# Optimization experiments

Measured on AMD Instinct MI355X. Metric: run time of the kernel, lower is better.

The kernel has to match this reference:

```python
import jax, jax.numpy as jnp
import numpy as np

NUM_EXPERTS = 8
TOP_K = 2
D = 2048   # hidden_dim
F = 4096   # ffn_dim


def setup_inputs() -> dict:
    key = jax.random.key(0)
    k0, k1, k2, k3, k4 = jax.random.split(key, 5)
    hidden_states = jax.random.normal(k0, (2, 2048, D), dtype=jnp.float32)
    gate_w = jax.random.normal(k1, (NUM_EXPERTS, D), dtype=jnp.float32) * 0.02
    w1 = jax.random.normal(k2, (NUM_EXPERTS, F, D), dtype=jnp.float32) * 0.02
    w2 = jax.random.normal(k3, (NUM_EXPERTS, D, F), dtype=jnp.float32) * 0.02
    w3 = jax.random.normal(k4, (NUM_EXPERTS, F, D), dtype=jnp.float32) * 0.02
    return {"hidden_states": hidden_states, "gate_w": gate_w, "w1": w1, "w2": w2, "w3": w3}


def reference(hidden_states, gate_w, w1, w2, w3):
    B, S, Dm = hidden_states.shape
    h = hidden_states.reshape(-1, Dm)                      # [T, D]
    router_logits = h @ gate_w.T                           # [T, E]
    rw = jax.nn.softmax(router_logits.astype(jnp.float32), axis=-1)
    rw, selected = jax.lax.top_k(rw, TOP_K)                # [T, K], [T, K]
    rw = rw / jnp.sum(rw, axis=-1, keepdims=True)
    rw = rw.astype(h.dtype)
    final = jnp.zeros_like(h)
    for e in range(NUM_EXPERTS):                            # small fixed loop over experts
        w = jnp.sum(rw * (selected == e), axis=1, keepdims=True)  # [T, 1]
        gated = jax.nn.silu(h @ w1[e].T) * (h @ w3[e].T)   # [T, F]
        final = final + (gated @ w2[e].T) * w              # [T, D]
    return final.reshape(B, S, Dm), router_logits
```

## Files before the change

### kernel.cpp

```cpp
#include <hip/hip_runtime.h>
#include <hip/hip_bf16.h>
#include <stdint.h>

#define NE 8
#define DD 2048
#define FF 4096
#define TT 4096
#define NRB 1024
#define NCV 3072

typedef __attribute__((ext_vector_type(8))) short bf16x8;
typedef __attribute__((ext_vector_type(4))) float f32x4;

__device__ inline unsigned short f2bf(float f) {
  union { float f; unsigned u; } x; x.f = f;
  unsigned r = x.u + 0x7fffu + ((x.u >> 16) & 1u);
  return (unsigned short)(r >> 16);
}
__device__ inline float bf2f(unsigned short v) {
  union { unsigned u; float f; } x; x.u = (unsigned)v << 16; return x.f;
}

__device__ __forceinline__ void convw(const float* __restrict__ src,
                                      unsigned short* __restrict__ dst,
                                      long base, int tid) {
  float4 v[16];
#pragma unroll
  for (int j = 0; j < 16; j++)
    v[j] = *(const float4*)(src + base + j * 1024 + tid * 4);
#pragma unroll
  for (int j = 0; j < 16; j++) {
    ushort4 o;
    o.x = f2bf(v[j].x); o.y = f2bf(v[j].y); o.z = f2bf(v[j].z); o.w = f2bf(v[j].w);
    *(ushort4*)(dst + base + j * 1024 + tid * 4) = o;
  }
}

#define GLL16(g, l) __builtin_amdgcn_global_load_lds( \
    (__attribute__((address_space(1))) void*)(void*)(g), \
    (__attribute__((address_space(3))) void*)(l), 16, 0, 0)

__device__ __forceinline__ void router_one(
    int t, int lane, const float* __restrict__ h, const float* __restrict__ gw,
    float* __restrict__ logits, unsigned short* __restrict__ hb,
    int* __restrict__ counts, int* __restrict__ tok_idx,
    int* __restrict__ sel_e, int* __restrict__ sel_slot, float* __restrict__ sel_w) {
  const float4* hr = (const float4*)(h + (size_t)t * DD);
  float4 hv[8];
  float acc[NE];
#pragma unroll
  for (int e = 0; e < NE; e++) acc[e] = 0.f;
#pragma unroll
  for (int j = 0; j < 8; j++) hv[j] = hr[j * 64 + lane];
  ushort4* hbr = (ushort4*)(hb + (size_t)t * DD);
#pragma unroll
  for (int j = 0; j < 8; j++) {
    ushort4 o;
    o.x = f2bf(hv[j].x); o.y = f2bf(hv[j].y); o.z = f2bf(hv[j].z); o.w = f2bf(hv[j].w);
    hbr[j * 64 + lane] = o;
  }
#pragma unroll
  for (int e = 0; e < NE; e++) {
    const float4* g = (const float4*)(gw + (size_t)e * DD);
    float a = 0.f;
#pragma unroll
    for (int j = 0; j < 8; j++) {
      float4 gv = g[j * 64 + lane];
      a += hv[j].x * gv.x + hv[j].y * gv.y + hv[j].z * gv.z + hv[j].w * gv.w;
    }
    acc[e] = a;
  }
#pragma unroll
  for (int e = 0; e < NE; e++) {
    float v = acc[e];
#pragma unroll
    for (int o = 32; o > 0; o >>= 1) v += __shfl_xor(v, o, 64);
    acc[e] = v;
  }
  if (lane == 0) {
#pragma unroll
    for (int e = 0; e < NE; e++) logits[(size_t)t * NE + e] = acc[e];
    int e1 = 0; float m1 = acc[0];
#pragma unroll
    for (int e = 1; e < NE; e++) if (acc[e] > m1) { m1 = acc[e]; e1 = e; }
    int e2 = -1; float m2 = -3.4e38f;
#pragma unroll
    for (int e = 0; e < NE; e++) if (e != e1 && acc[e] > m2) { m2 = acc[e]; e2 = e; }
    float s = expf(m2 - m1);
    float wa = 1.f / (1.f + s);
    float wb = s * wa;
    int s1 = atomicAdd(&counts[e1], 1);
    tok_idx[e1 * TT + s1] = t;
    int s2 = atomicAdd(&counts[e2], 1);
    tok_idx[e2 * TT + s2] = t;
    sel_e[2 * t] = e1; sel_slot[2 * t] = s1; sel_w[2 * t] = wa;
    sel_e[2 * t + 1] = e2; sel_slot[2 * t + 1] = s2; sel_w[2 * t + 1] = wb;
  }
}

__global__ __launch_bounds__(256) void prep_kernel(
    const float* __restrict__ h, const float* __restrict__ gw,
    float* __restrict__ logits, unsigned short* __restrict__ hb,
    int* __restrict__ counts, int* __restrict__ tok_idx,
    int* __restrict__ sel_e, int* __restrict__ sel_slot, float* __restrict__ sel_w,
    const float* __restrict__ w1, unsigned short* __restrict__ w1b,
    const float* __restrict__ w3, unsigned short* __restrict__ w3b,
    const float* __restrict__ w2, unsigned short* __restrict__ w2b) {
  int b = blockIdx.x;
  int tid = threadIdx.x;
  if (b < NRB) {
    router_one(b * 4 + (tid >> 6), tid & 63,
               h, gw, logits, hb, counts, tok_idx, sel_e, sel_slot, sel_w);
    return;
  }
  int cb = b - NRB;
  int t = cb >> 10;
  int lb = cb & 1023;
  const float* src = (t == 0) ? w1 : (t == 1) ? w3 : w2;
  unsigned short* dst = (t == 0) ? w1b : (t == 1) ? w3b : w2b;
#pragma unroll
  for (int it = 0; it < 4; it++) {
    long base = (long)(it * 1024 + lb) * 16384;
    convw(src, dst, base, tid);
  }
}

__global__ void offsets_kernel(const int* __restrict__ counts, int* __restrict__ offsets) {
  if (threadIdx.x == 0) {
    int r = 0;
    for (int e = 0; e < NE; e++) { offsets[e] = r; r += counts[e]; }
  }
}


__global__ __launch_bounds__(256) void gemm1_kernel(
    const unsigned short* __restrict__ w1b, const unsigned short* __restrict__ w3b,
    const unsigned short* __restrict__ hb, const int* __restrict__ tok_idx,
    const int* __restrict__ counts, const int* __restrict__ offsets,
    unsigned short* __restrict__ gated) {
  __shared__ __align__(16) char lds[32768];
  char* Ab = lds;
  char* B1 = lds + 16384;
  char* B3 = lds + 24576;

  int bid = blockIdx.x;
  int x = bid & 7;
  int rest = bid >> 3;
  int m = rest & 31;
  int q = rest >> 5;
  int p = x + 8 * q;
  int n = p & 63;
  int e = p >> 6;
  int cnt = counts[e];
  int row0 = m * 128;
  if (row0 >= cnt) return;
  int offe = offsets[e];
  int tid = threadIdx.x;

  long asrc[4];
#pragma unroll
  for (int i = 0; i < 4; i++) {
    int r = i * 32 + (tid >> 3);
    int rr = row0 + r; if (rr >= cnt) rr = cnt - 1;
    int tok = tok_idx[e * TT + rr];
    asrc[i] = (long)tok * DD + (((tid & 7) ^ (r & 7)) * 8);
  }
  int fbase = n * 64;
  long ebase = (long)e * FF * DD;
  long bsrc[2];
#pragma unroll
  for (int i = 0; i < 2; i++) {
    int r = i * 32 + (tid >> 3);
    bsrc[i] = ebase + (long)(fbase + r) * DD + (((tid & 7) ^ (r & 7)) * 8);
  }

  f32x4 acc1[4][2], acc3[4][2];
#pragma unroll
  for (int i = 0; i < 4; i++)
#pragma unroll
    for (int j = 0; j < 2; j++) { acc1[i][j] = (f32x4){0,0,0,0}; acc3[i][j] = (f32x4){0,0,0,0}; }

  int wv = tid >> 6;
  int lane = tid & 63;
  int wr = (wv >> 1) * 64;
  int wc = (wv & 1) * 32;
  int lrow = lane & 15;
  int lk4 = lane >> 4;

  for (int k0 = 0; k0 < DD; k0 += 64) {
    if (k0) __syncthreads();
#pragma unroll
    for (int i = 0; i < 4; i++)
      GLL16(hb + asrc[i] + k0, Ab + i * 4096 + tid * 16);
#pragma unroll
    for (int i = 0; i < 2; i++) {
      GLL16(w1b + bsrc[i] + k0, B1 + i * 4096 + tid * 16);
      GLL16(w3b + bsrc[i] + k0, B3 + i * 4096 + tid * 16);
    }
    __syncthreads();
#pragma unroll
    for (int kk = 0; kk < 2; kk++) {
      int kseg = kk * 4 + lk4;
      bf16x8 af[4], b1f[2], b3f[2];
#pragma unroll
      for (int i = 0; i < 4; i++) {
        int row = wr + i * 16 + lrow;
        af[i] = *(const bf16x8*)(Ab + row * 128 + ((kseg ^ (row & 7)) * 16));
      }
#pragma unroll
      for (int j = 0; j < 2; j++) {
        int row = wc + j * 16 + lrow;
        int off = row * 128 + ((kseg ^ (row & 7)) * 16);
        b1f[j] = *(const bf16x8*)(B1 + off);
        b3f[j] = *(const bf16x8*)(B3 + off);
      }
#pragma unroll
      for (int i = 0; i < 4; i++)
#pragma unroll
        for (int j = 0; j < 2; j++) {
          acc1[i][j] = __builtin_amdgcn_mfma_f32_16x16x32_bf16(af[i], b1f[j], acc1[i][j], 0, 0, 0);
          acc3[i][j] = __builtin_amdgcn_mfma_f32_16x16x32_bf16(af[i], b3f[j], acc3[i][j], 0, 0, 0);
        }
    }
  }
  int crow0 = wr + (lane >> 4) * 4;
  int ccol0 = wc + (lane & 15);
#pragma unroll
  for (int i = 0; i < 4; i++)
#pragma unroll
    for (int j = 0; j < 2; j++)
#pragma unroll
      for (int r = 0; r < 4; r++) {
        int trow = crow0 + i * 16 + r;
        if (row0 + trow < cnt) {
          float g = acc1[i][j][r];
          float sg = g / (1.f + __expf(-g));
          float val = sg * acc3[i][j][r];
          gated[(size_t)(offe + row0 + trow) * FF + (fbase + ccol0 + j * 16)] = f2bf(val);
        }
      }
}

__global__ __launch_bounds__(256) void gemm2_kernel(
    const unsigned short* __restrict__ w2b, const unsigned short* __restrict__ gated,
    const int* __restrict__ counts, const int* __restrict__ offsets,
    unsigned short* __restrict__ eout) {
  __shared__ __align__(16) char lds[32768];
  char* Ab = lds;
  char* Bb = lds + 16384;

  int bid = blockIdx.x;
  int x = bid & 7;
  int rest = bid >> 3;
  int m = rest & 31;
  int q = rest >> 5;
  int p = x + 8 * q;
  int n = p & 15;
  int e = p >> 4;
  int cnt = counts[e];
  int row0 = m * 128;
  if (row0 >= cnt) return;
  int offe = offsets[e];
  int tid = threadIdx.x;

  long asrc[4];
#pragma unroll
  for (int i = 0; i < 4; i++) {
    int r = i * 32 + (tid >> 3);
    int rr = row0 + r; if (rr >= cnt) rr = cnt - 1;
    asrc[i] = (long)(offe + rr) * FF + (((tid & 7) ^ (r & 7)) * 8);
  }
  int dbase = n * 128;
  long ebase = (long)e * DD * FF;
  long bsrc[4];
#pragma unroll
  for (int i = 0; i < 4; i++) {
    int r = i * 32 + (tid >> 3);
    bsrc[i] = ebase + (long)(dbase + r) * FF + (((tid & 7) ^ (r & 7)) * 8);
  }

  f32x4 acc[4][4];
#pragma unroll
  for (int i = 0; i < 4; i++)
#pragma unroll
    for (int j = 0; j < 4; j++) acc[i][j] = (f32x4){0,0,0,0};

  int wv = tid >> 6;
  int lane = tid & 63;
  int wr = (wv >> 1) * 64;
  int wc = (wv & 1) * 64;
  int lrow = lane & 15;
  int lk4 = lane >> 4;

  for (int k0 = 0; k0 < FF; k0 += 64) {
    if (k0) __syncthreads();
#pragma unroll
    for (int i = 0; i < 4; i++)
      GLL16(gated + asrc[i] + k0, Ab + i * 4096 + tid * 16);
#pragma unroll
    for (int i = 0; i < 4; i++)
      GLL16(w2b + bsrc[i] + k0, Bb + i * 4096 + tid * 16);
    __syncthreads();
#pragma unroll
    for (int kk = 0; kk < 2; kk++) {
      int kseg = kk * 4 + lk4;
      bf16x8 af[4], bf[4];
#pragma unroll
      for (int i = 0; i < 4; i++) {
        int row = wr + i * 16 + lrow;
        af[i] = *(const bf16x8*)(Ab + row * 128 + ((kseg ^ (row & 7)) * 16));
      }
#pragma unroll
      for (int j = 0; j < 4; j++) {
        int row = wc + j * 16 + lrow;
        bf[j] = *(const bf16x8*)(Bb + row * 128 + ((kseg ^ (row & 7)) * 16));
      }
#pragma unroll
      for (int i = 0; i < 4; i++)
#pragma unroll
        for (int j = 0; j < 4; j++)
          acc[i][j] = __builtin_amdgcn_mfma_f32_16x16x32_bf16(af[i], bf[j], acc[i][j], 0, 0, 0);
    }
  }
  int crow0 = wr + (lane >> 4) * 4;
  int ccol0 = wc + (lane & 15);
#pragma unroll
  for (int i = 0; i < 4; i++)
#pragma unroll
    for (int j = 0; j < 4; j++)
#pragma unroll
      for (int r = 0; r < 4; r++) {
        int trow = crow0 + i * 16 + r;
        if (row0 + trow < cnt)
          eout[(size_t)(offe + row0 + trow) * DD + (dbase + ccol0 + j * 16)] = f2bf(acc[i][j][r]);
      }
}

__global__ void gather_kernel(const unsigned short* __restrict__ eout, const int* __restrict__ offsets,
                              const int* __restrict__ sel_e, const int* __restrict__ sel_slot,
                              const float* __restrict__ sel_w, float* __restrict__ out) {
  int idx = blockIdx.x * 256 + threadIdx.x;
  int t = idx >> 8;
  int c = (idx & 255) * 8;
  int ea = sel_e[2 * t], eb = sel_e[2 * t + 1];
  long sa = (long)(offsets[ea] + sel_slot[2 * t]) * DD + c;
  long sb = (long)(offsets[eb] + sel_slot[2 * t + 1]) * DD + c;
  float wa = sel_w[2 * t], wb = sel_w[2 * t + 1];
  union { uint4 v; unsigned short h[8]; } va, vb;
  va.v = *(const uint4*)(eout + sa);
  vb.v = *(const uint4*)(eout + sb);
  float4 o0, o1;
  o0.x = wa * bf2f(va.h[0]) + wb * bf2f(vb.h[0]);
  o0.y = wa * bf2f(va.h[1]) + wb * bf2f(vb.h[1]);
  o0.z = wa * bf2f(va.h[2]) + wb * bf2f(vb.h[2]);
  o0.w = wa * bf2f(va.h[3]) + wb * bf2f(vb.h[3]);
  o1.x = wa * bf2f(va.h[4]) + wb * bf2f(vb.h[4]);
  o1.y = wa * bf2f(va.h[5]) + wb * bf2f(vb.h[5]);
  o1.z = wa * bf2f(va.h[6]) + wb * bf2f(vb.h[6]);
  o1.w = wa * bf2f(va.h[7]) + wb * bf2f(vb.h[7]);
  float* op = out + (size_t)t * DD + c;
  *(float4*)op = o0;
  *(float4*)(op + 4) = o1;
}

extern "C" void kernel_launch(void* const* d_in, const int* in_sizes, int n_in,
                              void* d_out, int out_size, void* d_ws, size_t ws_size,
                              hipStream_t stream) {
  const float* h  = (const float*)d_in[0];
  const float* gw = (const float*)d_in[1];
  const float* w1 = (const float*)d_in[2];
  const float* w2 = (const float*)d_in[3];
  const float* w3 = (const float*)d_in[4];
  float* out = (float*)d_out;
  float* logits = out + (size_t)TT * DD;

  char* wp = (char*)d_ws;
  int* counts = (int*)wp; wp += 256;
  int* offsets = (int*)wp; wp += 256;
  int* tok_idx = (int*)wp; wp += (size_t)NE * TT * 4;
  int* sel_e = (int*)wp; wp += (size_t)TT * 2 * 4;
  int* sel_slot = (int*)wp; wp += (size_t)TT * 2 * 4;
  float* sel_w = (float*)wp; wp += (size_t)TT * 2 * 4;
  unsigned short* hb = (unsigned short*)wp; wp += (size_t)TT * DD * 2;
  unsigned short* gated = (unsigned short*)wp; wp += (size_t)TT * 2 * FF * 2;
  unsigned short* eout = (unsigned short*)wp; wp += (size_t)TT * 2 * DD * 2;
  long nw = (long)NE * FF * DD;
  unsigned short* w1b = (unsigned short*)wp; wp += (size_t)nw * 2;
  unsigned short* w3b = (unsigned short*)wp; wp += (size_t)nw * 2;
  unsigned short* w2b = (unsigned short*)wp; wp += (size_t)nw * 2;
  if ((size_t)(wp - (char*)d_ws) > ws_size) return;

  hipMemsetAsync(counts, 0, 32, stream);
  prep_kernel<<<NRB + NCV, 256, 0, stream>>>(
      h, gw, logits, hb, counts, tok_idx, sel_e, sel_slot, sel_w,
      w1, w1b, w3, w3b, w2, w2b);
  offsets_kernel<<<1, 64, 0, stream>>>(counts, offsets);
  gemm1_kernel<<<8 * 32 * 64, 256, 0, stream>>>(w1b, w3b, hb, tok_idx, counts, offsets, gated);
  gemm2_kernel<<<8 * 32 * 16, 256, 0, stream>>>(w2b, gated, counts, offsets, eout);
  gather_kernel<<<TT * DD / 8 / 256, 256, 0, stream>>>(eout, offsets, sel_e, sel_slot, sel_w, out);
}
```

Baseline: 845.2 us.

## Split prep into router, weight-convert, and deterministic token-bucket build kernels

Replaces the fused prep kernel with separate router, weight-conversion and single-block bucket-build kernels. The per-token atomic expert counting is swapped for a block-wide prefix count, which gives a deterministic token order per expert and folds in the offsets computation. The weight conversion now uses a grid-stride pattern with 16-byte packed bf16 stores. It adds a kernel launch and a serial single-block scan, and the prefix loop is O(256) per thread.

```diff
diff --git a/kernel.cpp b/kernel.cpp
--- a/kernel.cpp
+++ b/kernel.cpp
@@ -6,8 +6,7 @@
 #define DD 2048
 #define FF 4096
 #define TT 4096
-#define NRB 1024
-#define NCV 3072
+#define NCVB 2048
 
 typedef __attribute__((ext_vector_type(8))) short bf16x8;
 typedef __attribute__((ext_vector_type(4))) float f32x4;
@@ -20,20 +19,11 @@
 __device__ inline float bf2f(unsigned short v) {
   union { unsigned u; float f; } x; x.u = (unsigned)v << 16; return x.f;
 }
-
-__device__ __forceinline__ void convw(const float* __restrict__ src,
-                                      unsigned short* __restrict__ dst,
-                                      long base, int tid) {
-  float4 v[16];
-#pragma unroll
-  for (int j = 0; j < 16; j++)
-    v[j] = *(const float4*)(src + base + j * 1024 + tid * 4);
-#pragma unroll
-  for (int j = 0; j < 16; j++) {
-    ushort4 o;
-    o.x = f2bf(v[j].x); o.y = f2bf(v[j].y); o.z = f2bf(v[j].z); o.w = f2bf(v[j].w);
-    *(ushort4*)(dst + base + j * 1024 + tid * 4) = o;
-  }
+__device__ inline uint4 pk8f(float4 a, float4 b) {
+  union { unsigned short h[8]; uint4 v; } o;
+  o.h[0] = f2bf(a.x); o.h[1] = f2bf(a.y); o.h[2] = f2bf(a.z); o.h[3] = f2bf(a.w);
+  o.h[4] = f2bf(b.x); o.h[5] = f2bf(b.y); o.h[6] = f2bf(b.z); o.h[7] = f2bf(b.w);
+  return o.v;
 }
 
 #define GLL16(g, l) __builtin_amdgcn_global_load_lds( \
@@ -43,8 +33,7 @@
 __device__ __forceinline__ void router_one(
     int t, int lane, const float* __restrict__ h, const float* __restrict__ gw,
     float* __restrict__ logits, unsigned short* __restrict__ hb,
-    int* __restrict__ counts, int* __restrict__ tok_idx,
-    int* __restrict__ sel_e, int* __restrict__ sel_slot, float* __restrict__ sel_w) {
+    int* __restrict__ sel_e, float* __restrict__ sel_w) {
   const float4* hr = (const float4*)(h + (size_t)t * DD);
   float4 hv[8];
   float acc[NE];
@@ -89,47 +78,84 @@
     float s = expf(m2 - m1);
     float wa = 1.f / (1.f + s);
     float wb = s * wa;
-    int s1 = atomicAdd(&counts[e1], 1);
-    tok_idx[e1 * TT + s1] = t;
-    int s2 = atomicAdd(&counts[e2], 1);
-    tok_idx[e2 * TT + s2] = t;
-    sel_e[2 * t] = e1; sel_slot[2 * t] = s1; sel_w[2 * t] = wa;
-    sel_e[2 * t + 1] = e2; sel_slot[2 * t + 1] = s2; sel_w[2 * t + 1] = wb;
-  }
-}
-
-__global__ __launch_bounds__(256) void prep_kernel(
+    sel_e[2 * t] = e1; sel_w[2 * t] = wa;
+    sel_e[2 * t + 1] = e2; sel_w[2 * t + 1] = wb;
+  }
+}
+
+__global__ __launch_bounds__(256) void router_kernel(
     const float* __restrict__ h, const float* __restrict__ gw,
     float* __restrict__ logits, unsigned short* __restrict__ hb,
-    int* __restrict__ counts, int* __restrict__ tok_idx,
-    int* __restrict__ sel_e, int* __restrict__ sel_slot, float* __restrict__ sel_w,
+    int* __restrict__ sel_e, float* __restrict__ sel_w) {
+  router_one(blockIdx.x * 4 + (threadIdx.x >> 6), threadIdx.x & 63,
+             h, gw, logits, hb, sel_e, sel_w);
+}
+
+__global__ __launch_bounds__(256) void build_kernel(
+    const int* __restrict__ sel_e, int* __restrict__ counts, int* __restrict__ offsets,
+    int* __restrict__ tok_idx, int* __restrict__ sel_slot) {
+  __shared__ int cnt[256][NE];
+  int tid = threadIdx.x;
+  int le[32];
+#pragma unroll
+  for (int k = 0; k < 32; k++) le[k] = sel_e[tid * 32 + k];
+  int c[NE];
+#pragma unroll
+  for (int e = 0; e < NE; e++) c[e] = 0;
+#pragma unroll
+  for (int k = 0; k < 32; k++) c[le[k]]++;
+#pragma unroll
+  for (int e = 0; e < NE; e++) cnt[tid][e] = c[e];
+  __syncthreads();
+  int pre[NE];
+#pragma unroll
+  for (int e = 0; e < NE; e++) pre[e] = 0;
+  for (int i = 0; i < tid; i++)
+#pragma unroll
+    for (int e = 0; e < NE; e++) pre[e] += cnt[i][e];
+  if (tid == 255) {
+    int r = 0;
+#pragma unroll
+    for (int e = 0; e < NE; e++) {
+      int tot = pre[e] + c[e];
+      counts[e] = tot; offsets[e] = r; r += tot;
+    }
+  }
+  int base_t = tid * 16;
+#pragma unroll
+  for (int k = 0; k < 32; k++) {
+    int e = le[k];
+    int s = pre[e]++;
+    tok_idx[e * TT + s] = base_t + (k >> 1);
+    sel_slot[tid * 32 + k] = s;
+  }
+}
+
+__device__ __forceinline__ void conv_stream(const float* __restrict__ src,
+                                            unsigned short* __restrict__ dst,
+                                            long i0, long stride) {
+#pragma unroll
+  for (int it = 0; it < 8; it++) {
+    long g0 = (i0 + (long)(2 * it) * stride) * 8;
+    long g1 = g0 + stride * 8;
+    float4 a0 = *(const float4*)(src + g0);
+    float4 a1 = *(const float4*)(src + g0 + 4);
+    float4 b0 = *(const float4*)(src + g1);
+    float4 b1 = *(const float4*)(src + g1 + 4);
+    *(uint4*)(dst + g0) = pk8f(a0, a1);
+    *(uint4*)(dst + g1) = pk8f(b0, b1);
+  }
+}
+
+__global__ __launch_bounds__(256) void convert_kernel(
     const float* __restrict__ w1, unsigned short* __restrict__ w1b,
     const float* __restrict__ w3, unsigned short* __restrict__ w3b,
     const float* __restrict__ w2, unsigned short* __restrict__ w2b) {
-  int b = blockIdx.x;
-  int tid = threadIdx.x;
-  if (b < NRB) {
-    router_one(b * 4 + (tid >> 6), tid & 63,
-               h, gw, logits, hb, counts, tok_idx, sel_e, sel_slot, sel_w);
-    return;
-  }
-  int cb = b - NRB;
-  int t = cb >> 10;
-  int lb = cb & 1023;
-  const float* src = (t == 0) ? w1 : (t == 1) ? w3 : w2;
-  unsigned short* dst = (t == 0) ? w1b : (t == 1) ? w3b : w2b;
-#pragma unroll
-  for (int it = 0; it < 4; it++) {
-    long base = (long)(it * 1024 + lb) * 16384;
-    convw(src, dst, base, tid);
-  }
-}
-
-__global__ void offsets_kernel(const int* __restrict__ counts, int* __restrict__ offsets) {
-  if (threadIdx.x == 0) {
-    int r = 0;
-    for (int e = 0; e < NE; e++) { offsets[e] = r; r += counts[e]; }
-  }
+  long i0 = (long)blockIdx.x * 256 + threadIdx.x;
+  long stride = (long)NCVB * 256;
+  conv_stream(w1, w1b, i0, stride);
+  conv_stream(w3, w3b, i0, stride);
+  conv_stream(w2, w2b, i0, stride);
 }
 
 
@@ -390,11 +416,9 @@
   unsigned short* w2b = (unsigned short*)wp; wp += (size_t)nw * 2;
   if ((size_t)(wp - (char*)d_ws) > ws_size) return;
 
-  hipMemsetAsync(counts, 0, 32, stream);
-  prep_kernel<<<NRB + NCV, 256, 0, stream>>>(
-      h, gw, logits, hb, counts, tok_idx, sel_e, sel_slot, sel_w,
-      w1, w1b, w3, w3b, w2, w2b);
-  offsets_kernel<<<1, 64, 0, stream>>>(counts, offsets);
+  router_kernel<<<TT / 4, 256, 0, stream>>>(h, gw, logits, hb, sel_e, sel_w);
+  convert_kernel<<<NCVB, 256, 0, stream>>>(w1, w1b, w3, w3b, w2, w2b);
+  build_kernel<<<1, 256, 0, stream>>>(sel_e, counts, offsets, tok_idx, sel_slot);
   gemm1_kernel<<<8 * 32 * 64, 256, 0, stream>>>(w1b, w3b, hb, tok_idx, counts, offsets, gated);
   gemm2_kernel<<<8 * 32 * 16, 256, 0, stream>>>(w2b, gated, counts, offsets, eout);
   gather_kernel<<<TT * DD / 8 / 256, 256, 0, stream>>>(eout, offsets, sel_e, sel_slot, sel_w, out);
```

Measured after the change: 778.5 us. 1.09x faster.
